# Kernel optimization log

Measured on AMD Instinct MI355X. Metric: run time of the kernel, lower is better.

The kernel has to match this reference:

```python
import jax, jax.numpy as jnp
import numpy as np

B, T = 4, 15
NY = NX = 256
RES = 0.05
LAT0 = 32.0
G = 9.81
F0 = 1e-4
C0 = 2.7
DT = 21600.0
TINT = 86400.0
NSTEP = int(TINT // DT)  # 4 Euler sub-steps

# --- grid spacing: mean of dx, dy as in lonlat2dxdy (uniform lon/lat grid) ---
_lat = LAT0 + RES * np.arange(NX, dtype=np.float64)  # lat varies along axis 1
_dx_mean = RES * 111000.0
_dy_mean = RES * 111000.0 * np.mean(np.cos(np.deg2rad(_lat)))
DX = np.float32(0.5 * (_dx_mean + _dy_mean))

# --- Helmholtz operator in DST-I space, shape (NY-2, NX-2) (square grid) ---
_i = np.arange(1, NX - 1, dtype=np.float64)
_j = np.arange(1, NY - 1, dtype=np.float64)
_X, _Y = np.meshgrid(_i, _j, indexing='ij')
_lap = (2 * (np.cos(np.pi / (NX - 1) * _X) - 1) / DX**2
        + 2 * (np.cos(np.pi / (NY - 1) * _Y) - 1) / DX**2)
HELM = jnp.asarray((G / F0) * _lap - G * F0 / C0**2, dtype=jnp.float32)

# --- boundary masks (SSH=None -> no NaN land mask; ind0 is empty) ---
_m = np.full((NY, NX), 3, dtype=np.int32)
_m[0, :] = _m[:, 0] = _m[-1, :] = _m[:, -1] = 1
_m[1, 1:-1] = 2; _m[1:-1, 1] = 2
_m[-2, 1:-1] = 2; _m[-3, 1:-1] = 2
_m[1:-1, -2] = 2; _m[1:-1, -3] = 2
IND12 = jnp.asarray((_m == 1) | (_m == 2))


def dstI1D(x):
    """1D type-I discrete sine transform along last axis."""
    n = x.shape[-1]
    xp = jnp.pad(x, [(0, 0)] * (x.ndim - 1) + [(1, 1)])
    return jnp.fft.irfft(-1j * xp, norm='ortho')[..., 1:n + 1]


def dstI2D(x):
    return jnp.swapaxes(dstI1D(jnp.swapaxes(dstI1D(x), -1, -2)), -1, -2)


def h2uv(h):
    """SSH -> geostrophic (u, v). f is the constant F0."""
    u = jnp.zeros_like(h).at[..., 1:-1, 1:].set(
        -G / F0 * (h[..., 2:, :-1] + h[..., 2:, 1:] - h[..., :-2, 1:] - h[..., :-2, :-1]) / (4 * DX))
    v = jnp.zeros_like(h).at[..., 1:, 1:-1].set(
        G / F0 * (h[..., 1:, 2:] + h[..., :-1, 2:] - h[..., :-1, :-2] - h[..., 1:, :-2]) / (4 * DX))
    return u, v


def h2pv(h, hbc):
    """SSH -> potential vorticity with boundary values from hbc on ind1|ind2."""
    interior = (G / F0 * ((h[..., 2:, 1:-1] + h[..., :-2, 1:-1] - 2 * h[..., 1:-1, 1:-1]) / DX**2
                          + (h[..., 1:-1, 2:] + h[..., 1:-1, :-2] - 2 * h[..., 1:-1, 1:-1]) / DX**2)
                - G * F0 / C0**2 * h[..., 1:-1, 1:-1])
    q = jnp.zeros_like(h).at[..., 1:-1, 1:-1].set(interior)
    return jnp.where(IND12, -G * F0 / C0**2 * hbc, q)


def _adv(up, vp, um, vm, v0):
    """3rd-order upwind advection."""
    c = 1.0 / (6 * DX)
    inner = (
        -up[..., 1:-1, 1:-1] * c * (2 * v0[..., 2:-2, 3:-1] + 3 * v0[..., 2:-2, 2:-2] - 6 * v0[..., 2:-2, 1:-3] + v0[..., 2:-2, :-4])
        + um[..., 1:-1, 1:-1] * c * (v0[..., 2:-2, 4:] - 6 * v0[..., 2:-2, 3:-1] + 3 * v0[..., 2:-2, 2:-2] + 2 * v0[..., 2:-2, 1:-3])
        - vp[..., 1:-1, 1:-1] * c * (2 * v0[..., 3:-1, 2:-2] + 3 * v0[..., 2:-2, 2:-2] - 6 * v0[..., 1:-3, 2:-2] + v0[..., :-4, 2:-2])
        + vm[..., 1:-1, 1:-1] * c * (v0[..., 4:, 2:-2] - 6 * v0[..., 3:-1, 2:-2] + 3 * v0[..., 2:-2, 2:-2] + 2 * v0[..., 1:-3, 2:-2]))
    return jnp.zeros_like(v0).at[..., 2:-2, 2:-2].set(inner)


def rhs(u, v, q0, way=1.0):
    uT = way * 0.5 * (u[..., 1:-1, 1:-1] + u[..., 1:-1, 2:])
    vT = way * 0.5 * (v[..., 1:-1, 1:-1] + v[..., 2:, 1:-1])
    up = jnp.maximum(uT, 0.0); um = jnp.minimum(uT, 0.0)
    vp = jnp.maximum(vT, 0.0); vm = jnp.minimum(vT, 0.0)
    r = _adv(up, vp, um, vm, q0)
    # beta term is identically zero: f = F0 is spatially constant. Kdiffus=None.
    return jnp.where(IND12, 0.0, r)


def pv2h(q, hb, qb):
    """PV -> SSH via DST-based inverse Helmholtz solve."""
    qin = q[..., 1:-1, 1:-1] - qb[..., 1:-1, 1:-1]
    inv = dstI2D(dstI2D(qin) / HELM)
    return jnp.zeros_like(q).at[..., 1:-1, 1:-1].set(inv) + hb


def conv2d(x, w, b):
    y = jax.lax.conv_general_dilated(x, w, (1, 1), 'SAME',
                                     dimension_numbers=('NCHW', 'OIHW', 'NCHW'))
    return y + b[None, :, None, None]


def qg_forecast(x):
    """One-day QG forecast of each frame from the previous one (NSTEP Euler sub-steps)."""
    h0 = x[:, :-1]            # [B, T-1, NY, NX]
    hb = h0                    # background / boundary SSH
    qb = h2pv(hb, hb)

    def body(carry, _):
        h, q = carry
        u, v = h2uv(h)
        q1 = q + DT * rhs(u, v, q)
        h1 = pv2h(q1, hb, qb)
        return (h1, q1), None

    (hf, _), _ = jax.lax.scan(body, (h0, qb), None, length=NSTEP)
    return hf


def setup_inputs() -> dict:
    key = jax.random.key(0)
    ks = jax.random.split(key, 8)
    s = 0.05
    return {
        'x': jax.random.normal(ks[0], (B, T, NY, NX), jnp.float32),
        'w_in': s * jax.random.normal(ks[1], (64, T, 3, 3), jnp.float32),
        'b_in': jnp.zeros((64,), jnp.float32),
        'w_hid': s * jax.random.normal(ks[2], (64, 64, 3, 3), jnp.float32),
        'b_hid': jnp.zeros((64,), jnp.float32),
        'w_b1': s * jax.random.normal(ks[3], (64, 64, 3, 3), jnp.float32),
        'b_b1': jnp.zeros((64,), jnp.float32),
        'w_b21': s * jax.random.normal(ks[4], (64, 64, 3, 3), jnp.float32),
        'b_b21': jnp.zeros((64,), jnp.float32),
        'w_b22': s * jax.random.normal(ks[5], (64, 64, 3, 3), jnp.float32),
        'b_b22': jnp.zeros((64,), jnp.float32),
        'w_out': s * jax.random.normal(ks[6], (T, 128, 3, 3), jnp.float32),
        'b_out': jnp.zeros((T,), jnp.float32),
    }


def reference(x, w_in, b_in, w_hid, b_hid, w_b1, b_b1, w_b21, b_b21,
              w_b22, b_b22, w_out, b_out):
    # QG dynamical prior cost
    hf = qg_forecast(x)
    dyn_cost = jnp.mean((x[:, 1:] - hf) ** 2)
    # bilinear AE prior cost (bilin_quad=False -> product of two branches)
    z = conv2d(x, w_in, b_in)
    z = conv2d(jax.nn.relu(z), w_hid, b_hid)
    nonlin = conv2d(z, w_b21, b_b21) * conv2d(z, w_b22, b_b22)
    xa = conv2d(jnp.concatenate([conv2d(z, w_b1, b_b1), nonlin], axis=1), w_out, b_out)
    ae_cost = jnp.mean((x - xa) ** 2)
    return dyn_cost + ae_cost
```

## Files before the change

### kernel.cpp

```cpp
#include <hip/hip_runtime.h>
#include <math.h>

#define NS 56
#define NPIX 65536

static constexpr double D_PI = 3.14159265358979323846;

typedef __attribute__((ext_vector_type(8))) short short8;
typedef __attribute__((ext_vector_type(4))) float f32x4;
typedef __attribute__((ext_vector_type(16))) float f32x16;

__device__ inline unsigned short f2bf(float f) {
  union { float f; unsigned int u; } v; v.f = f;
  unsigned int r = v.u + 0x7FFFu + ((v.u >> 16) & 1u);
  return (unsigned short)(r >> 16);
}
__device__ inline float bf2f(unsigned short b) {
  union { float f; unsigned int u; } v; v.u = ((unsigned int)b) << 16;
  return v.f;
}

#define SLC      (NS * NPIX)
#define OFF_PART 0
#define OFF_CNT  3584
#define OFF_S    4096
#define OFF_HM   36864
#define OFF_H    102400
#define OFF_QB   (OFF_H + SLC)
#define OFF_DQ0  (OFF_QB + SLC)
#define OFF_DQ1  (OFF_DQ0 + SLC / 2)
#define OFF_A1   (OFF_DQ1 + SLC / 2)
#define OFF_XP   (OFF_A1 + SLC / 2)
#define OFF_Z1   (OFF_XP + 2097152)
#define OFF_Z2   (OFF_Z1 + 8388608)
#define OFF_BC   (OFF_Z2 + 8388608)
#define OFF_XA   (OFF_BC + 8388608)
#define OFF_WT   (OFF_XA + 2097152)
#define W_IN    0
#define W_HID   10240
#define W_B1    47104
#define W_B21   83968
#define W_B22   120832
#define W_O1    157696
#define W_O2    166912

#define QCLAMP 1.0e12f
#define HCLAMP 1.0e15f

__global__ __launch_bounds__(256) void k_preamble(const float* __restrict__ x,
                                                  const float* __restrict__ w_in,
                                                  const float* __restrict__ w_hid,
                                                  const float* __restrict__ w_b1,
                                                  const float* __restrict__ w_b21,
                                                  const float* __restrict__ w_b22,
                                                  const float* __restrict__ w_out,
                                                  unsigned short* __restrict__ S,
                                                  float* __restrict__ HM,
                                                  unsigned short* __restrict__ wtb,
                                                  float* __restrict__ h,
                                                  float* __restrict__ qb,
                                                  unsigned short* __restrict__ xp,
                                                  unsigned int* __restrict__ cnt,
                                                  float dx2, float gf, float gfc) {
  const int blk = blockIdx.x;
  const int tid = threadIdx.x;
  if (blk < 256) {
    int idx = blk * 256 + tid;
    if (idx == 0) *cnt = 0u;
    int i = idx >> 8, j = idx & 255;
    float sv = 0.f, hv = 1.f;
    if (i < 254 && j < 254) {
      double arg = D_PI * (double)((i + 1) * (j + 1)) / 255.0;
      sv = (float)((2.0 / sqrt(510.0)) * sin(arg));
      double la = 2.0 * (cos(D_PI * (double)(i + 1) / 255.0) - 1.0) / (double)dx2
                + 2.0 * (cos(D_PI * (double)(j + 1) / 255.0) - 1.0) / (double)dx2;
      hv = (float)((9.81 / 1e-4) * la - 9.81 * 1e-4 / (2.7 * 2.7));
    }
    S[idx] = f2bf(sv);
    HM[idx] = hv;
  } else if (blk < 256 + 1008) {
    int jb = blk - 256;
    int job = jb / 144;
    int e = (jb - job * 144) * 256 + tid;
    const float* src;
    int dstOff, chunks, icpShift, icw, ic0, icReal, ocw, ocReal;
    switch (job) {
      case 0: src = w_in;  dstOff = W_IN;  chunks = 5;  icpShift = 4; icw = 15;  ic0 = 0;  icReal = 15; ocw = 64; ocReal = 64; break;
      case 1: src = w_hid; dstOff = W_HID; chunks = 18; icpShift = 6; icw = 64;  ic0 = 0;  icReal = 64; ocw = 64; ocReal = 64; break;
      case 2: src = w_b1;  dstOff = W_B1;  chunks = 18; icpShift = 6; icw = 64;  ic0 = 0;  icReal = 64; ocw = 64; ocReal = 64; break;
      case 3: src = w_b21; dstOff = W_B21; chunks = 18; icpShift = 6; icw = 64;  ic0 = 0;  icReal = 64; ocw = 64; ocReal = 64; break;
      case 4: src = w_b22; dstOff = W_B22; chunks = 18; icpShift = 6; icw = 64;  ic0 = 0;  icReal = 64; ocw = 64; ocReal = 64; break;
      case 5: src = w_out; dstOff = W_O1;  chunks = 18; icpShift = 6; icw = 128; ic0 = 0;  icReal = 64; ocw = 16; ocReal = 15; break;
      default: src = w_out; dstOff = W_O2; chunks = 18; icpShift = 6; icw = 128; ic0 = 64; icReal = 64; ocw = 16; ocReal = 15; break;
    }
    int total = chunks * 4 * ocw * 8;
    if (e < total) {
      int j = e & 7;
      int oc = (e >> 3) % ocw;
      int ckg = e / (8 * ocw);
      int kg = ckg & 3, c = ckg >> 2;
      int Kidx = c * 32 + kg * 8 + j;
      int tap = Kidx >> icpShift;
      int ic = Kidx & ((1 << icpShift) - 1);
      float v = 0.f;
      if (tap < 9 && ic < icReal && oc < ocReal)
        v = src[((size_t)oc * icw + ic0 + ic) * 9 + tap];
      wtb[dstOff + e] = f2bf(v);
    }
  } else if (blk < 256 + 1008 + 14336) {
    int idx = (blk - 1264) * 256 + tid;
    int s = idx >> 16, p = idx & 65535;
    int y = p >> 8, xx = p & 255;
    int b = s / 14, t = s - b * 14;
    const float* hb = x + (size_t)(b * 15 + t) * NPIX;
    float hc = hb[p];
    float qv;
    if (y >= 2 && y <= 252 && xx >= 2 && xx <= 252) {
      qv = gf * ((hb[p + 256] + hb[p - 256] - 2.f * hc) / dx2
               + (hb[p + 1] + hb[p - 1] - 2.f * hc) / dx2) - gfc * hc;
    } else {
      qv = -gfc * hc;
    }
    h[idx] = hc;
    qb[idx] = qv;
  } else {
    int e = (blk - 15600) * 256 + tid;
    int b = e >> 16, p = e & 65535;
    const float* xb = x + (size_t)b * 15 * NPIX + p;
    union { unsigned short u16[16]; uint4 u4[2]; } vv;
#pragma unroll
    for (int c = 0; c < 15; ++c) vv.u16[c] = f2bf(xb[(size_t)c * NPIX]);
    vv.u16[15] = 0;
    uint4* dst = (uint4*)&xp[(size_t)e * 16];
    dst[0] = vv.u4[0];
    dst[1] = vv.u4[1];
  }
}

template <bool FIRST>
__global__ __launch_bounds__(256) void k_qrhs_dq(const float* __restrict__ h,
                                                 const float* __restrict__ qbb,
                                                 const unsigned short* __restrict__ dqin,
                                                 unsigned short* __restrict__ dqout,
                                                 float ngf, float pgf, float fdx,
                                                 float cc, float dtf) {
  int idx = blockIdx.x * 256 + threadIdx.x;
  int s = idx >> 16, p = idx & 65535;
  int y = p >> 8, xx = p & 255;
  const float* H = h + (size_t)s * NPIX;
  const float* QB = qbb + (size_t)s * NPIX;
  const unsigned short* DQ = dqin + (size_t)s * NPIX;
  const int base = p - 257;
  auto dqv = [&](int d) -> float {
    if (FIRST) return 0.f;
    return bf2f(DQ[(base + d) & 65535]);
  };
  float q1mqb = 0.f;
  if (y >= 2 && y <= 252 && xx >= 2 && xx <= 252) {
    float hSW = H[p + 255], hS = H[p + 256], hSE = H[p + 257];
    float hNW = H[p - 257], hN = H[p - 256], hNE = H[p - 255];
    float hW = H[p - 1], hE = H[p + 1];
    float uA = ngf * (hSW + hS - hN - hNW) / fdx;
    float uB = ngf * (hS + hSE - hNE - hN) / fdx;
    float vA = pgf * (hE + hNE - hNW - hW) / fdx;
    float vB = pgf * (hSE + hE - hW - hSW) / fdx;
    float uT = 0.5f * (uA + uB);
    float vT = 0.5f * (vA + vB);
    float up = fmaxf(uT, 0.f), um = fminf(uT, 0.f);
    float vp = fmaxf(vT, 0.f), vm = fminf(vT, 0.f);
    float qbc = QB[p];
    float Q0 = qbc + dqv(0);
    float QE = QB[p + 1] + dqv(1), QW = QB[p - 1] + dqv(-1);
    float QEE = QB[p + 2] + dqv(2), QWW = QB[p - 2] + dqv(-2);
    float QS = QB[p + 256] + dqv(256), QN = QB[p - 256] + dqv(-256);
    float QSS = QB[p + 512] + dqv(512), QNN = QB[p - 512] + dqv(-512);
    float r = -up * cc * (2.f * QE + 3.f * Q0 - 6.f * QW + QWW)
            + um * cc * (QEE - 6.f * QE + 3.f * Q0 + 2.f * QW)
            - vp * cc * (2.f * QS + 3.f * Q0 - 6.f * QN + QNN)
            + vm * cc * (QSS - 6.f * QS + 3.f * Q0 + 2.f * QN);
    float q1 = Q0 + dtf * r;
    q1 = fminf(fmaxf(q1, -QCLAMP), QCLAMP);
    q1mqb = q1 - qbc;
  }
  int wy = (y == 0) ? 254 : ((y == 255) ? 255 : y - 1);
  int wx = (xx == 0) ? 254 : ((xx == 255) ? 255 : xx - 1);
  dqout[(size_t)s * NPIX + wy * 256 + wx] = f2bf(q1mqb);
}

template <int EPI>
__global__ __launch_bounds__(512) void k_solve(const unsigned short* __restrict__ Sm,
                                               const unsigned short* __restrict__ Xb,
                                               unsigned short* __restrict__ Ob,
                                               const float* __restrict__ HM,
                                               const float* __restrict__ xin,
                                               float* __restrict__ hout) {
  __shared__ unsigned short Ul[32 * 256];
  const int s = blockIdx.x, q = blockIdx.y;
  const unsigned short* X = Xb + (size_t)s * NPIX;
  const int lane = threadIdx.x & 63, w = threadIdx.x >> 6;
  const int r31 = lane & 31, kh = lane >> 5;

  f32x16 acc;
#pragma unroll
  for (int i = 0; i < 16; ++i) acc[i] = 0.f;
  {
    const int ar = (32 * q + r31) * 256;
    const int br = (32 * w + r31) * 256;
#pragma unroll 4
    for (int kc = 0; kc < 256; kc += 16) {
      short8 a = *(const short8*)&Sm[ar + kc + kh * 8];
      short8 b = *(const short8*)&X[br + kc + kh * 8];
      acc = __builtin_amdgcn_mfma_f32_32x32x16_bf16(a, b, acc, 0, 0, 0);
    }
  }
  {
    const int col = 32 * w + r31;
    const int g = col >> 3, c7 = col & 7;
#pragma unroll
    for (int reg = 0; reg < 16; ++reg) {
      int i = (reg & 3) + 8 * (reg >> 2) + 4 * kh;
      Ul[i * 256 + (((g ^ (i & 7)) << 3) | c7)] = f2bf(acc[reg]);
    }
  }
  __syncthreads();

  f32x16 acc2;
#pragma unroll
  for (int i = 0; i < 16; ++i) acc2[i] = 0.f;
  {
    const int ar = (32 * w + r31) * 256;
    const int urow = r31 * 256;
    const int x7 = (r31 & 7);
#pragma unroll 4
    for (int kc = 0; kc < 256; kc += 16) {
      int g0 = (kc >> 3) + kh;
      short8 a = *(const short8*)&Sm[ar + kc + kh * 8];
      short8 b = *(const short8*)&Ul[urow + ((g0 ^ x7) << 3)];
      acc2 = __builtin_amdgcn_mfma_f32_32x32x16_bf16(a, b, acc2, 0, 0, 0);
    }
  }
  const int gn = 32 * q + r31;
  if (EPI == 0) {
    unsigned short* O = Ob + (size_t)s * NPIX;
#pragma unroll
    for (int reg = 0; reg < 16; ++reg) {
      int gm = 32 * w + (reg & 3) + 8 * (reg >> 2) + 4 * kh;
      O[(size_t)gm * 256 + gn] = f2bf(acc2[reg] / HM[(size_t)gm * 256 + gn]);
    }
  } else {
    int b = s / 14, t = s - b * 14;
    const float* hb = xin + (size_t)(b * 15 + t) * NPIX;
    float* H = hout + (size_t)s * NPIX;
    if (gn < 254) {
#pragma unroll
      for (int reg = 0; reg < 16; ++reg) {
        int gm = 32 * w + (reg & 3) + 8 * (reg >> 2) + 4 * kh;
        if (gm < 254) {
          size_t o = (size_t)(gm + 1) * 256 + (gn + 1);
          float hv = acc2[reg] + hb[o];
          H[o] = fminf(fmaxf(hv, -HCLAMP), HCLAMP);
        }
      }
    }
  }
}

template <bool RELU, int EMODE>
__global__ __launch_bounds__(512) void k_conv64b(const unsigned short* __restrict__ in,
                                                 const unsigned short* __restrict__ wt,
                                                 const float* __restrict__ bias,
                                                 const unsigned short* __restrict__ other,
                                                 unsigned short* __restrict__ out) {
  __shared__ unsigned short tile[324 * 64];
  const int tid = threadIdx.x;
  const int lane = tid & 63, wave = tid >> 6;
  const int cl = lane & 15, kg = lane >> 4;
  const int wrow = wave & 3, wh = wave >> 2;
  const int b = blockIdx.z;
  const int gx0 = blockIdx.x * 16, gy0 = blockIdx.y * 16;

  f32x4 acc[4][2];
#pragma unroll
  for (int j = 0; j < 2; ++j) {
    float bv = bias[wh * 32 + j * 16 + cl];
#pragma unroll
    for (int i = 0; i < 4; ++i) acc[i][j] = (f32x4){bv, bv, bv, bv};
  }

  const unsigned short* inb = in + (size_t)b * NPIX * 64;
  for (int c = tid; c < 2592; c += 512) {
    int pp = c >> 3, g = c & 7;
    int ly = pp / 18, lx = pp - ly * 18;
    int iy = gy0 + ly - 1, ix = gx0 + lx - 1;
    uint4 v = make_uint4(0u, 0u, 0u, 0u);
    if (iy >= 0 && iy < 256 && ix >= 0 && ix < 256)
      v = *(const uint4*)&inb[((size_t)iy * 256 + ix) * 64 + g * 8];
    int sw = g ^ (pp & 7);
    *(uint4*)&tile[pp * 64 + sw * 8] = v;
  }
  __syncthreads();

#pragma unroll 3
  for (int cm = 0; cm < 18; ++cm) {
    const int tap = cm >> 1;
    const int g = (cm & 1) * 4 + kg;
    const int dy = tap / 3, dxx = tap - dy * 3;
    short8 bfr[2];
#pragma unroll
    for (int j = 0; j < 2; ++j)
      bfr[j] = *(const short8*)&wt[(((size_t)cm * 4 + kg) * 64 + wh * 32 + j * 16 + cl) * 8];
    const int tc = cl + dxx;
#pragma unroll
    for (int i = 0; i < 4; ++i) {
      int pp = (wrow * 4 + i + dy) * 18 + tc;
      int g2 = g ^ (pp & 7);
      short8 av = *(const short8*)&tile[pp * 64 + g2 * 8];
#pragma unroll
      for (int j = 0; j < 2; ++j)
        acc[i][j] = __builtin_amdgcn_mfma_f32_16x16x32_bf16(av, bfr[j], acc[i][j], 0, 0, 0);
    }
  }

  const size_t outBase = (size_t)b * NPIX * 64;
#pragma unroll
  for (int i = 0; i < 4; ++i) {
    int y = gy0 + wrow * 4 + i;
#pragma unroll
    for (int j = 0; j < 2; ++j) {
      int oc = wh * 32 + j * 16 + cl;
#pragma unroll
      for (int r = 0; r < 4; ++r) {
        int px = gx0 + kg * 4 + r;
        size_t oi = outBase + ((size_t)y * 256 + px) * 64 + oc;
        float v = acc[i][j][r];
        if (EMODE == 1) v *= bf2f(other[oi]);
        if (RELU) v = fmaxf(v, 0.f);
        out[oi] = f2bf(v);
      }
    }
  }
}

__global__ __launch_bounds__(512) void k_convmul(const unsigned short* __restrict__ in,
                                                 const unsigned short* __restrict__ wtA,
                                                 const unsigned short* __restrict__ wtB,
                                                 const float* __restrict__ biasA,
                                                 const float* __restrict__ biasB,
                                                 unsigned short* __restrict__ out) {
  __shared__ unsigned short tile[324 * 64];
  const int tid = threadIdx.x;
  const int lane = tid & 63, wave = tid >> 6;
  const int cl = lane & 15, kg = lane >> 4;
  const int wrow = wave & 3, wh = wave >> 2;
  const int b = blockIdx.z;
  const int gx0 = blockIdx.x * 16, gy0 = blockIdx.y * 16;

  f32x4 accA[4][2], accB[4][2];
#pragma unroll
  for (int j = 0; j < 2; ++j) {
    float ba = biasA[wh * 32 + j * 16 + cl], bb = biasB[wh * 32 + j * 16 + cl];
#pragma unroll
    for (int i = 0; i < 4; ++i) {
      accA[i][j] = (f32x4){ba, ba, ba, ba};
      accB[i][j] = (f32x4){bb, bb, bb, bb};
    }
  }

  const unsigned short* inb = in + (size_t)b * NPIX * 64;
  for (int c = tid; c < 2592; c += 512) {
    int pp = c >> 3, g = c & 7;
    int ly = pp / 18, lx = pp - ly * 18;
    int iy = gy0 + ly - 1, ix = gx0 + lx - 1;
    uint4 v = make_uint4(0u, 0u, 0u, 0u);
    if (iy >= 0 && iy < 256 && ix >= 0 && ix < 256)
      v = *(const uint4*)&inb[((size_t)iy * 256 + ix) * 64 + g * 8];
    int sw = g ^ (pp & 7);
    *(uint4*)&tile[pp * 64 + sw * 8] = v;
  }
  __syncthreads();

#pragma unroll 2
  for (int cm = 0; cm < 18; ++cm) {
    const int tap = cm >> 1;
    const int g = (cm & 1) * 4 + kg;
    const int dy = tap / 3, dxx = tap - dy * 3;
    const int tc = cl + dxx;
    short8 wa[2], wb[2];
#pragma unroll
    for (int j = 0; j < 2; ++j) {
      wa[j] = *(const short8*)&wtA[(((size_t)cm * 4 + kg) * 64 + wh * 32 + j * 16 + cl) * 8];
      wb[j] = *(const short8*)&wtB[(((size_t)cm * 4 + kg) * 64 + wh * 32 + j * 16 + cl) * 8];
    }
#pragma unroll
    for (int i = 0; i < 4; ++i) {
      int pp = (wrow * 4 + i + dy) * 18 + tc;
      int g2 = g ^ (pp & 7);
      short8 av = *(const short8*)&tile[pp * 64 + g2 * 8];
#pragma unroll
      for (int j = 0; j < 2; ++j) {
        accA[i][j] = __builtin_amdgcn_mfma_f32_16x16x32_bf16(av, wa[j], accA[i][j], 0, 0, 0);
        accB[i][j] = __builtin_amdgcn_mfma_f32_16x16x32_bf16(av, wb[j], accB[i][j], 0, 0, 0);
      }
    }
  }

  const size_t outBase = (size_t)b * NPIX * 64;
#pragma unroll
  for (int i = 0; i < 4; ++i) {
    int y = gy0 + wrow * 4 + i;
#pragma unroll
    for (int j = 0; j < 2; ++j) {
      int oc = wh * 32 + j * 16 + cl;
#pragma unroll
      for (int r = 0; r < 4; ++r) {
        int px = gx0 + kg * 4 + r;
        size_t oi = outBase + ((size_t)y * 256 + px) * 64 + oc;
        out[oi] = f2bf(accA[i][j][r] * accB[i][j][r]);
      }
    }
  }
}

__global__ __launch_bounds__(512) void k_convout(const unsigned short* __restrict__ in0,
                                                 const unsigned short* __restrict__ in1,
                                                 const unsigned short* __restrict__ wt,
                                                 const float* __restrict__ bias,
                                                 unsigned short* __restrict__ out) {
  __shared__ unsigned short tile[324 * 64];
  const int tid = threadIdx.x;
  const int lane = tid & 63, wave = tid >> 6;
  const int cl = lane & 15, kg = lane >> 4;
  const int b = blockIdx.z;
  const int gx0 = blockIdx.x * 16, gy0 = blockIdx.y * 16;

  f32x4 acc[2];
  {
    float bv = (cl < 15) ? bias[cl] : 0.f;
    acc[0] = (f32x4){bv, bv, bv, bv};
    acc[1] = acc[0];
  }

  for (int src = 0; src < 2; ++src) {
    const unsigned short* inb = (src ? in1 : in0) + (size_t)b * NPIX * 64;
    const unsigned short* wtp = wt + src * 9216;
    if (src) __syncthreads();
    for (int c = tid; c < 2592; c += 512) {
      int pp = c >> 3, g = c & 7;
      int ly = pp / 18, lx = pp - ly * 18;
      int iy = gy0 + ly - 1, ix = gx0 + lx - 1;
      uint4 v = make_uint4(0u, 0u, 0u, 0u);
      if (iy >= 0 && iy < 256 && ix >= 0 && ix < 256)
        v = *(const uint4*)&inb[((size_t)iy * 256 + ix) * 64 + g * 8];
      int sw = g ^ (pp & 7);
      *(uint4*)&tile[pp * 64 + sw * 8] = v;
    }
    __syncthreads();
#pragma unroll 3
    for (int cm = 0; cm < 18; ++cm) {
      const int tap = cm >> 1;
      const int g = (cm & 1) * 4 + kg;
      const int dy = tap / 3, dxx = tap - dy * 3;
      short8 bfr = *(const short8*)&wtp[(((size_t)cm * 4 + kg) * 16 + cl) * 8];
      const int tc = cl + dxx;
#pragma unroll
      for (int i = 0; i < 2; ++i) {
        int pp = (wave * 2 + i + dy) * 18 + tc;
        int g2 = g ^ (pp & 7);
        short8 av = *(const short8*)&tile[pp * 64 + g2 * 8];
        acc[i] = __builtin_amdgcn_mfma_f32_16x16x32_bf16(av, bfr, acc[i], 0, 0, 0);
      }
    }
  }

  const size_t outBase = (size_t)b * NPIX * 16;
#pragma unroll
  for (int i = 0; i < 2; ++i) {
    int y = gy0 + wave * 2 + i;
#pragma unroll
    for (int r = 0; r < 4; ++r) {
      int px = gx0 + kg * 4 + r;
      size_t oi = outBase + ((size_t)y * 256 + px) * 16 + cl;
      out[oi] = f2bf(acc[i][r]);
    }
  }
}

__global__ __launch_bounds__(256) void k_conv16(const unsigned short* __restrict__ in,
                                                const unsigned short* __restrict__ wt,
                                                const float* __restrict__ bias,
                                                unsigned short* __restrict__ out) {
  __shared__ unsigned short wlds[10240];
  __shared__ unsigned short tile[324 * 16];

  const int tid = threadIdx.x;
  const int lane = tid & 63, wave = tid >> 6;
  const int cl = lane & 15, kg = lane >> 4;
  const int b = blockIdx.z;
  const int gx0 = blockIdx.x * 16, gy0 = blockIdx.y * 16;

  {
    uint4* wl = (uint4*)wlds;
    const uint4* wg = (const uint4*)wt;
    for (int i = tid; i < 1280; i += 256) wl[i] = wg[i];
  }
  const unsigned short* inb = in + (size_t)b * NPIX * 16;
  for (int c = tid; c < 648; c += 256) {
    int pp = c >> 1, g = c & 1;
    int ly = pp / 18, lx = pp - ly * 18;
    int iy = gy0 + ly - 1, ix = gx0 + lx - 1;
    uint4 v = make_uint4(0u, 0u, 0u, 0u);
    if (iy >= 0 && iy < 256 && ix >= 0 && ix < 256)
      v = *(const uint4*)&inb[((size_t)iy * 256 + ix) * 16 + g * 8];
    int sw = g ^ (pp & 1);
    *(uint4*)&tile[pp * 16 + sw * 8] = v;
  }
  __syncthreads();

  f32x4 acc[4][4];
#pragma unroll
  for (int j = 0; j < 4; ++j) {
    float bv = bias[j * 16 + cl];
#pragma unroll
    for (int i = 0; i < 4; ++i) acc[i][j] = (f32x4){bv, bv, bv, bv};
  }

#pragma unroll
  for (int c = 0; c < 5; ++c) {
    int tap = 2 * c + (kg >> 1);
    int dy = tap / 3, dxx = tap - dy * 3;
    int gidx = kg & 1;
    short8 bfr[4];
#pragma unroll
    for (int j = 0; j < 4; ++j)
      bfr[j] = *(const short8*)&wlds[((c * 4 + kg) * 64 + j * 16 + cl) * 8];
    int tc = cl + dxx;
#pragma unroll
    for (int i = 0; i < 4; ++i) {
      int tr = wave * 4 + i + dy;
      if (tr > 17) tr = 17;
      int pp = tr * 18 + tc;
      int g2 = gidx ^ (pp & 1);
      short8 av = *(const short8*)&tile[pp * 16 + g2 * 8];
#pragma unroll
      for (int j = 0; j < 4; ++j)
        acc[i][j] = __builtin_amdgcn_mfma_f32_16x16x32_bf16(av, bfr[j], acc[i][j], 0, 0, 0);
    }
  }

  const size_t outBase = (size_t)b * NPIX * 64;
#pragma unroll
  for (int i = 0; i < 4; ++i) {
    int y = gy0 + wave * 4 + i;
#pragma unroll
    for (int j = 0; j < 4; ++j) {
      int oc = j * 16 + cl;
#pragma unroll
      for (int r = 0; r < 4; ++r) {
        int px = gx0 + kg * 4 + r;
        size_t oi = outBase + ((size_t)y * 256 + px) * 64 + oc;
        out[oi] = f2bf(fmaxf(acc[i][j][r], 0.f));
      }
    }
  }
}

__global__ __launch_bounds__(256) void k_red_all(const float* __restrict__ x,
                                                 const float* __restrict__ h,
                                                 const unsigned short* __restrict__ xa,
                                                 double* __restrict__ part,
                                                 unsigned int* __restrict__ cnt,
                                                 float* __restrict__ out) {
  const int NB1 = 1024, NBT = 1536;
  const int bid = blockIdx.x;
  const int tid = threadIdx.x;
  double sum = 0.0;
  if (bid < NB1) {
    for (int e = bid * 256 + tid; e < NS * NPIX; e += NB1 * 256) {
      int s = e >> 16, p = e & 65535;
      int b = s / 14, t = s - b * 14;
      float d = x[(size_t)(b * 15 + t + 1) * NPIX + p] - h[e];
      sum += (double)d * (double)d;
    }
  } else {
    for (int e = (bid - NB1) * 256 + tid; e < 60 * NPIX; e += (NBT - NB1) * 256) {
      int b = e / (15 * NPIX);
      int r2 = e - b * 15 * NPIX;
      int c = r2 >> 16, p = r2 & 65535;
      float xav = bf2f(xa[((size_t)b * NPIX + p) * 16 + c]);
      float d = x[e] - xav;
      sum += (double)d * (double)d;
    }
  }
  for (int o = 32; o > 0; o >>= 1) sum += __shfl_down(sum, o);
  __shared__ double sw[4];
  __shared__ bool last;
  int lane = tid & 63, wid = tid >> 6;
  if (lane == 0) sw[wid] = sum;
  __syncthreads();
  if (tid == 0) {
    part[bid] = sw[0] + sw[1] + sw[2] + sw[3];
    __threadfence();
    unsigned int t = atomicAdd(cnt, 1u);
    last = (t == (unsigned)(NBT - 1));
  }
  __syncthreads();
  if (last) {
    __threadfence();
    double s1 = 0.0, s2 = 0.0;
    for (int i = tid; i < NBT; i += 256) {
      if (i < NB1) s1 += part[i]; else s2 += part[i];
    }
    for (int o = 32; o > 0; o >>= 1) {
      s1 += __shfl_down(s1, o);
      s2 += __shfl_down(s2, o);
    }
    __shared__ double a1[4], a2[4];
    if (lane == 0) { a1[wid] = s1; a2[wid] = s2; }
    __syncthreads();
    if (tid == 0) {
      double v = (a1[0] + a1[1] + a1[2] + a1[3]) / (double)(NS * NPIX)
               + (a2[0] + a2[1] + a2[2] + a2[3]) / (double)(60 * NPIX);
      if (!(v == v)) v = 0.0;
      if (v > 1.0e30) v = 1.0e30;
      if (v < -1.0e30) v = -1.0e30;
      out[0] = (float)v;
    }
  }
}

extern "C" void kernel_launch(void* const* d_in, const int* in_sizes, int n_in,
                              void* d_out, int out_size, void* d_ws, size_t ws_size,
                              hipStream_t stream) {
  (void)in_sizes; (void)n_in; (void)out_size; (void)ws_size;
  const float* x     = (const float*)d_in[0];
  const float* w_in  = (const float*)d_in[1];
  const float* b_in  = (const float*)d_in[2];
  const float* w_hid = (const float*)d_in[3];
  const float* b_hid = (const float*)d_in[4];
  const float* w_b1  = (const float*)d_in[5];
  const float* b_b1  = (const float*)d_in[6];
  const float* w_b21 = (const float*)d_in[7];
  const float* b_b21 = (const float*)d_in[8];
  const float* w_b22 = (const float*)d_in[9];
  const float* b_b22 = (const float*)d_in[10];
  const float* w_out = (const float*)d_in[11];
  const float* b_out = (const float*)d_in[12];
  float* ws = (float*)d_ws;
  float* out = (float*)d_out;

  double mc = 0.0;
  for (int k = 0; k < 256; ++k) mc += cos((32.0 + 0.05 * k) * D_PI / 180.0);
  mc /= 256.0;
  float DXf = (float)(0.5 * (5550.0 + 5550.0 * mc));
  float dx2 = DXf * DXf;
  float gf  = (float)(9.81 / 1e-4);
  float ngf = (float)(-9.81 / 1e-4);
  float gfc = (float)(9.81 * 1e-4 / (2.7 * 2.7));
  float fdx = 4.0f * DXf;
  float cc  = 1.0f / (6.0f * DXf);
  float dtf = 21600.0f;

  double* part = (double*)d_ws;
  unsigned int* cnt = (unsigned int*)(ws + OFF_CNT);
  unsigned short* S  = (unsigned short*)(ws + OFF_S);
  float* HM = ws + OFF_HM;
  float* h  = ws + OFF_H;
  float* qb = ws + OFF_QB;
  unsigned short* dq0 = (unsigned short*)(ws + OFF_DQ0);
  unsigned short* dq1 = (unsigned short*)(ws + OFF_DQ1);
  unsigned short* A1 = (unsigned short*)(ws + OFF_A1);
  unsigned short* xp = (unsigned short*)(ws + OFF_XP);
  unsigned short* z1 = (unsigned short*)(ws + OFF_Z1);
  unsigned short* z2 = (unsigned short*)(ws + OFF_Z2);
  unsigned short* bc = (unsigned short*)(ws + OFF_BC);
  unsigned short* xa = (unsigned short*)(ws + OFF_XA);
  unsigned short* wtb = (unsigned short*)(ws + OFF_WT);

  k_preamble<<<dim3(16624), dim3(256), 0, stream>>>(x, w_in, w_hid, w_b1, w_b21, w_b22,
                                                    w_out, S, HM, wtb, h, qb, xp, cnt,
                                                    dx2, gf, gfc);

  dim3 sg(56, 8);
  dim3 qg(NS * NPIX / 256);
  unsigned short* dqc = dq0;
  unsigned short* dqn = dq1;
  for (int step = 0; step < 4; ++step) {
    if (step == 0)
      k_qrhs_dq<true><<<qg, dim3(256), 0, stream>>>(h, qb, dq1, dqc, ngf, gf, fdx, cc, dtf);
    else {
      k_qrhs_dq<false><<<qg, dim3(256), 0, stream>>>(h, qb, dqc, dqn, ngf, gf, fdx, cc, dtf);
      unsigned short* tmp = dqc; dqc = dqn; dqn = tmp;
    }
    k_solve<0><<<sg, dim3(512), 0, stream>>>(S, dqc, A1, HM, nullptr, nullptr);
    k_solve<1><<<sg, dim3(512), 0, stream>>>(S, A1, nullptr, nullptr, x, h);
  }

  dim3 cg4(16, 16, 4);
  k_conv16<<<cg4, dim3(256), 0, stream>>>(xp, wtb + W_IN, b_in, z1);
  k_conv64b<false, 0><<<cg4, dim3(512), 0, stream>>>(z1, wtb + W_HID, b_hid, nullptr, z2);
  k_conv64b<false, 0><<<cg4, dim3(512), 0, stream>>>(z2, wtb + W_B1, b_b1, nullptr, z1);
  k_convmul<<<cg4, dim3(512), 0, stream>>>(z2, wtb + W_B21, wtb + W_B22, b_b21, b_b22, bc);
  k_convout<<<cg4, dim3(512), 0, stream>>>(z1, bc, wtb + W_O1, b_out, xa);

  k_red_all<<<dim3(1536), dim3(256), 0, stream>>>(x, h, xa, part, cnt, out);
}
```

Before: 505.0 us.

## Fuse dynamical cost reduction into final solve epilogue and vectorize AE reduction

The last Helmholtz solve step now uses a new epilogue that computes the squared error against x[t+1] directly from the accumulators and writes per-block partial sums. It skips storing h to global memory. Border pixels, which are never updated by the solve, have their error computed by extra preamble blocks. The final reduction kernel now handles only the AE term, reading the packed bf16 xa with vector loads per pixel. This removes a full pass over h and x, at the cost of a more complex partial-sum indexing scheme shared across three kernels.

```diff
diff --git a/kernel.cpp b/kernel.cpp
--- a/kernel.cpp
+++ b/kernel.cpp
@@ -61,6 +61,7 @@
                                                   float* __restrict__ qb,
                                                   unsigned short* __restrict__ xp,
                                                   unsigned int* __restrict__ cnt,
+                                                  double* __restrict__ part,
                                                   float dx2, float gf, float gfc) {
   const int blk = blockIdx.x;
   const int tid = threadIdx.x;
@@ -123,7 +124,7 @@
     }
     h[idx] = hc;
     qb[idx] = qv;
-  } else {
+  } else if (blk < 256 + 1008 + 14336 + 1024) {
     int e = (blk - 15600) * 256 + tid;
     int b = e >> 16, p = e & 65535;
     const float* xb = x + (size_t)b * 15 * NPIX + p;
@@ -134,6 +135,28 @@
     uint4* dst = (uint4*)&xp[(size_t)e * 16];
     dst[0] = vv.u4[0];
     dst[1] = vv.u4[1];
+  } else {
+    int s = blk - 16624;
+    int b = s / 14, t = s - b * 14;
+    const float* hb = x + (size_t)(b * 15 + t) * NPIX;
+    const float* x1 = x + (size_t)(b * 15 + t + 1) * NPIX;
+    double sum = 0.0;
+    for (int i = tid; i < 1020; i += 256) {
+      int y, xc;
+      if (i < 256)      { y = 0;         xc = i; }
+      else if (i < 512) { y = 255;       xc = i - 256; }
+      else if (i < 766) { y = i - 511;   xc = 0; }
+      else              { y = i - 765;   xc = 255; }
+      int p = y * 256 + xc;
+      float d = x1[p] - hb[p];
+      sum += (double)d * (double)d;
+    }
+    for (int o = 32; o > 0; o >>= 1) sum += __shfl_down(sum, o);
+    __shared__ double sw[4];
+    int lane = tid & 63, wid = tid >> 6;
+    if (lane == 0) sw[wid] = sum;
+    __syncthreads();
+    if (tid == 0) part[1472 + s] = sw[0] + sw[1] + sw[2] + sw[3];
   }
 }
 
@@ -193,7 +216,8 @@
                                                unsigned short* __restrict__ Ob,
                                                const float* __restrict__ HM,
                                                const float* __restrict__ xin,
-                                               float* __restrict__ hout) {
+                                               float* __restrict__ hout,
+                                               double* __restrict__ part) {
   __shared__ unsigned short Ul[32 * 256];
   const int s = blockIdx.x, q = blockIdx.y;
   const unsigned short* X = Xb + (size_t)s * NPIX;
@@ -247,7 +271,7 @@
       int gm = 32 * w + (reg & 3) + 8 * (reg >> 2) + 4 * kh;
       O[(size_t)gm * 256 + gn] = f2bf(acc2[reg] / HM[(size_t)gm * 256 + gn]);
     }
-  } else {
+  } else if (EPI == 1) {
     int b = s / 14, t = s - b * 14;
     const float* hb = xin + (size_t)(b * 15 + t) * NPIX;
     float* H = hout + (size_t)s * NPIX;
@@ -261,6 +285,34 @@
           H[o] = fminf(fmaxf(hv, -HCLAMP), HCLAMP);
         }
       }
+    }
+  } else {
+    int b = s / 14, t = s - b * 14;
+    const float* hb = xin + (size_t)(b * 15 + t) * NPIX;
+    const float* x1 = xin + (size_t)(b * 15 + t + 1) * NPIX;
+    double dsum = 0.0;
+    if (gn < 254) {
+#pragma unroll
+      for (int reg = 0; reg < 16; ++reg) {
+        int gm = 32 * w + (reg & 3) + 8 * (reg >> 2) + 4 * kh;
+        if (gm < 254) {
+          size_t o = (size_t)(gm + 1) * 256 + (gn + 1);
+          float hv = acc2[reg] + hb[o];
+          hv = fminf(fmaxf(hv, -HCLAMP), HCLAMP);
+          float d = x1[o] - hv;
+          dsum += (double)d * (double)d;
+        }
+      }
+    }
+    for (int o = 32; o > 0; o >>= 1) dsum += __shfl_down(dsum, o);
+    __shared__ double sred[8];
+    if (lane == 0) sred[w] = dsum;
+    __syncthreads();
+    if (threadIdx.x == 0) {
+      double t8 = 0.0;
+#pragma unroll
+      for (int i = 0; i < 8; ++i) t8 += sred[i];
+      part[1024 + s * 8 + q] = t8;
     }
   }
 }
@@ -564,32 +616,26 @@
   }
 }
 
-__global__ __launch_bounds__(256) void k_red_all(const float* __restrict__ x,
-                                                 const float* __restrict__ h,
-                                                 const unsigned short* __restrict__ xa,
-                                                 double* __restrict__ part,
-                                                 unsigned int* __restrict__ cnt,
-                                                 float* __restrict__ out) {
-  const int NB1 = 1024, NBT = 1536;
+__global__ __launch_bounds__(256) void k_red_ae(const float* __restrict__ x,
+                                                const unsigned short* __restrict__ xa,
+                                                double* __restrict__ part,
+                                                unsigned int* __restrict__ cnt,
+                                                float* __restrict__ out) {
+  const int NBT = 1024;
   const int bid = blockIdx.x;
   const int tid = threadIdx.x;
+  const int e = bid * 256 + tid;
+  const int b = e >> 16, p = e & 65535;
+  union { unsigned short u16[16]; uint4 u4[2]; } vv;
+  const uint4* xap = (const uint4*)&xa[(size_t)e * 16];
+  vv.u4[0] = xap[0];
+  vv.u4[1] = xap[1];
+  const float* xb = x + (size_t)b * 15 * NPIX + p;
   double sum = 0.0;
-  if (bid < NB1) {
-    for (int e = bid * 256 + tid; e < NS * NPIX; e += NB1 * 256) {
-      int s = e >> 16, p = e & 65535;
-      int b = s / 14, t = s - b * 14;
-      float d = x[(size_t)(b * 15 + t + 1) * NPIX + p] - h[e];
-      sum += (double)d * (double)d;
-    }
-  } else {
-    for (int e = (bid - NB1) * 256 + tid; e < 60 * NPIX; e += (NBT - NB1) * 256) {
-      int b = e / (15 * NPIX);
-      int r2 = e - b * 15 * NPIX;
-      int c = r2 >> 16, p = r2 & 65535;
-      float xav = bf2f(xa[((size_t)b * NPIX + p) * 16 + c]);
-      float d = x[e] - xav;
-      sum += (double)d * (double)d;
-    }
+#pragma unroll
+  for (int c = 0; c < 15; ++c) {
+    float d = xb[(size_t)c * NPIX] - bf2f(vv.u16[c]);
+    sum += (double)d * (double)d;
   }
   for (int o = 32; o > 0; o >>= 1) sum += __shfl_down(sum, o);
   __shared__ double sw[4];
@@ -607,9 +653,8 @@
   if (last) {
     __threadfence();
     double s1 = 0.0, s2 = 0.0;
-    for (int i = tid; i < NBT; i += 256) {
-      if (i < NB1) s1 += part[i]; else s2 += part[i];
-    }
+    for (int i = tid; i < 504; i += 256) s1 += part[1024 + i];
+    for (int i = tid; i < NBT; i += 256) s2 += part[i];
     for (int o = 32; o > 0; o >>= 1) {
       s1 += __shfl_down(s1, o);
       s2 += __shfl_down(s2, o);
@@ -676,9 +721,9 @@
   unsigned short* xa = (unsigned short*)(ws + OFF_XA);
   unsigned short* wtb = (unsigned short*)(ws + OFF_WT);
 
-  k_preamble<<<dim3(16624), dim3(256), 0, stream>>>(x, w_in, w_hid, w_b1, w_b21, w_b22,
+  k_preamble<<<dim3(16680), dim3(256), 0, stream>>>(x, w_in, w_hid, w_b1, w_b21, w_b22,
                                                     w_out, S, HM, wtb, h, qb, xp, cnt,
-                                                    dx2, gf, gfc);
+                                                    part, dx2, gf, gfc);
 
   dim3 sg(56, 8);
   dim3 qg(NS * NPIX / 256);
@@ -691,8 +736,11 @@
       k_qrhs_dq<false><<<qg, dim3(256), 0, stream>>>(h, qb, dqc, dqn, ngf, gf, fdx, cc, dtf);
       unsigned short* tmp = dqc; dqc = dqn; dqn = tmp;
     }
-    k_solve<0><<<sg, dim3(512), 0, stream>>>(S, dqc, A1, HM, nullptr, nullptr);
-    k_solve<1><<<sg, dim3(512), 0, stream>>>(S, A1, nullptr, nullptr, x, h);
+    k_solve<0><<<sg, dim3(512), 0, stream>>>(S, dqc, A1, HM, nullptr, nullptr, part);
+    if (step < 3)
+      k_solve<1><<<sg, dim3(512), 0, stream>>>(S, A1, nullptr, nullptr, x, h, part);
+    else
+      k_solve<2><<<sg, dim3(512), 0, stream>>>(S, A1, nullptr, nullptr, x, nullptr, part);
   }
 
   dim3 cg4(16, 16, 4);
@@ -702,5 +750,5 @@
   k_convmul<<<cg4, dim3(512), 0, stream>>>(z2, wtb + W_B21, wtb + W_B22, b_b21, b_b22, bc);
   k_convout<<<cg4, dim3(512), 0, stream>>>(z1, bc, wtb + W_O1, b_out, xa);
 
-  k_red_all<<<dim3(1536), dim3(256), 0, stream>>>(x, h, xa, part, cnt, out);
-}
+  k_red_ae<<<dim3(1024), dim3(256), 0, stream>>>(x, xa, part, cnt, out);
+}
```

New measurement: 488.4 us. 1.03x faster.
